# Kernel tuning notes

Measured on AMD Instinct MI355X. Metric: run time of the kernel, lower is better.

The kernel has to match this reference:

```python
import jax, jax.numpy as jnp
import numpy as np

EMB, BS, H = 512, 1024, 8
HD = EMB // H
B, L = 8, 1024
EPS = 1e-5

def setup_inputs() -> dict:
    key = jax.random.key(0)
    ks = jax.random.split(key, 12)
    s = EMB ** -0.5
    return {
        "x": jax.random.normal(ks[0], (B, L, EMB), jnp.float32),
        "ln_g": jnp.ones((EMB,), jnp.float32),
        "ln_b": jnp.zeros((EMB,), jnp.float32),
        "Wq": jax.random.normal(ks[1], (EMB, EMB), jnp.float32) * s,
        "bq": jnp.zeros((EMB,), jnp.float32),
        "Wk": jax.random.normal(ks[2], (EMB, EMB), jnp.float32) * s,
        "bk": jnp.zeros((EMB,), jnp.float32),
        "Wv": jax.random.normal(ks[3], (EMB, EMB), jnp.float32) * s,
        "bv": jnp.zeros((EMB,), jnp.float32),
        "Wo": jax.random.normal(ks[4], (EMB, EMB), jnp.float32) * s,
        "bo": jnp.zeros((EMB,), jnp.float32),
        "Er": jax.random.normal(ks[5], (H, BS, HD), jnp.float32),
    }

def reference(x, ln_g, ln_b, Wq, bq, Wk, bk, Wv, bv, Wo, bo, Er):
    b, l, d = x.shape
    # LayerNorm
    mu = jnp.mean(x, axis=-1, keepdims=True)
    var = jnp.mean((x - mu) ** 2, axis=-1, keepdims=True)
    h = (x - mu) * jax.lax.rsqrt(var + EPS) * ln_g + ln_b
    # projections -> (B, H, L, HD)
    def split_heads(t):
        return t.reshape(b, l, H, HD).transpose(0, 2, 1, 3)
    q = split_heads(h @ Wq + bq)
    k = split_heads(h @ Wk + bk)
    v = split_heads(h @ Wv + bv)
    scores = jnp.einsum('bhld,bhkd->bhlk', q, k) * (HD ** -0.5)
    # relative bias: QEr_all[b,h,l,r] = q . Er[h,r]; then gather r = (k - l) mod BS
    QEr_all = jnp.einsum('bhld,hrd->bhlr', q, Er)  # (B,H,L,BS)
    rel = (jnp.arange(l)[None, :] - jnp.arange(l)[:, None]) % BS  # (L,L), torch negative-index wrap
    QEr = jnp.take_along_axis(QEr_all, rel[None, None], axis=-1)  # (B,H,L,L)
    w = jax.nn.softmax(scores + QEr, axis=-1)
    out = jnp.einsum('bhlk,bhkd->bhld', w, v)
    out = out.transpose(0, 2, 1, 3).reshape(b, l, d)
    return out @ Wo + bo
```

## Files before the change

kernel.cpp:

```cpp
#include <hip/hip_runtime.h>
#include <hip/hip_bf16.h>


typedef __bf16 bf16;
typedef __bf16 bf16x8 __attribute__((ext_vector_type(8)));
typedef float floatx4 __attribute__((ext_vector_type(4)));
typedef float f32x4 __attribute__((ext_vector_type(4)));

#define MFMA16 __builtin_amdgcn_mfma_f32_16x16x32_bf16

#define KS 72
#define PSS 72
#define GS 40
#define TS 72

__global__ __launch_bounds__(256) void prep_ln_kernel(
    const float* __restrict__ Wq, const float* __restrict__ Wk,
    const float* __restrict__ Wv, const float* __restrict__ Wo,
    const float* __restrict__ Er,
    const float* __restrict__ x, const float* __restrict__ g,
    const float* __restrict__ bvec,
    bf16* __restrict__ wt, bf16* __restrict__ er_b, bf16* __restrict__ h) {
  __shared__ __align__(16) bf16 T[64 * TS];
  int blk = blockIdx.x;
  int tid = threadIdx.x;
  if (blk < 256) {
    int w = blk >> 6, rem = blk & 63;
    int r0 = (rem >> 3) << 6, c0 = (rem & 7) << 6;
    const float* W = (w == 0) ? Wq : (w == 1) ? Wk : (w == 2) ? Wv : Wo;
    int row = tid >> 2, cc = (tid & 3) << 4;
    const f32x4* src = (const f32x4*)(W + (r0 + row) * 512 + c0 + cc);
#pragma unroll
    for (int q2 = 0; q2 < 4; q2++) {
      f32x4 v = src[q2];
#pragma unroll
      for (int j = 0; j < 4; j++)
        T[(cc + q2 * 4 + j) * TS + row] = (bf16)v[j];
    }
    __syncthreads();
    int nloc = tid >> 2, kc = (tid & 3) << 4;
    bf16x8 a = *(const bf16x8*)(T + nloc * TS + kc);
    bf16x8 b = *(const bf16x8*)(T + nloc * TS + kc + 8);
    bf16* dst = wt + (w << 18) + (c0 + nloc) * 512 + r0 + kc;
    *(bf16x8*)dst = a;
    *(bf16x8*)(dst + 8) = b;
    return;
  }
  if (blk < 2304) {
    int e = (blk - 256) * 256 + tid;
    er_b[e] = (bf16)Er[e];
    return;
  }
  int row = (blk - 2304) * 4 + (tid >> 6);
  int lane = tid & 63;
  const f32x4* xr = (const f32x4*)(x + row * 512 + lane * 8);
  f32x4 v0 = xr[0], v1 = xr[1];
  float f[8] = {v0[0], v0[1], v0[2], v0[3], v1[0], v1[1], v1[2], v1[3]};
  float s = 0.f, ss = 0.f;
#pragma unroll
  for (int i = 0; i < 8; i++) { s += f[i]; ss += f[i] * f[i]; }
#pragma unroll
  for (int m = 1; m < 64; m <<= 1) { s += __shfl_xor(s, m); ss += __shfl_xor(ss, m); }
  float mean = s * (1.0f / 512.0f);
  float var = ss * (1.0f / 512.0f) - mean * mean;
  float inv = rsqrtf(var + 1e-5f);
  const f32x4* gr = (const f32x4*)(g + lane * 8);
  const f32x4* br = (const f32x4*)(bvec + lane * 8);
  f32x4 g0 = gr[0], g1 = gr[1], b0 = br[0], b1 = br[1];
  float gg[8] = {g0[0], g0[1], g0[2], g0[3], g1[0], g1[1], g1[2], g1[3]};
  float bb[8] = {b0[0], b0[1], b0[2], b0[3], b1[0], b1[1], b1[2], b1[3]};
  bf16x8 o;
#pragma unroll
  for (int i = 0; i < 8; i++)
    o[i] = (bf16)((f[i] - mean) * inv * gg[i] + bb[i]);
  *(bf16x8*)(h + row * 512 + lane * 8) = o;
}


__global__ __launch_bounds__(256) void qkv_gemm(
    const bf16* __restrict__ A,
    const bf16* __restrict__ wt,
    const float* __restrict__ bq, const float* __restrict__ bk,
    const float* __restrict__ bv,
    bf16* __restrict__ q_ws, bf16* __restrict__ k_ws, bf16* __restrict__ vt_ws) {
  __shared__ __align__(16) bf16 smem[64 * 264];
  bf16* As = smem;
  bf16* Bs = smem + 128 * GS;
  int m0 = blockIdx.x * 128;
  int ng0 = blockIdx.y * 128;
  int w = ng0 >> 9;
  int n0 = ng0 & 511;
  const bf16* Bt = wt + (w << 18);
  int tid = threadIdx.x;
  int wave = tid >> 6, lane = tid & 63, quad = lane >> 4, l16 = lane & 15;
  int mq = (wave >> 1) * 64, nq = (wave & 1) * 64;

  floatx4 acc[4][4] = {};
  for (int k0 = 0; k0 < 512; k0 += 32) {
    int r = tid >> 1, c = (tid & 1) * 16;
    *(bf16x8*)(As + r * GS + c)     = *(const bf16x8*)(A + (m0 + r) * 512 + k0 + c);
    *(bf16x8*)(As + r * GS + c + 8) = *(const bf16x8*)(A + (m0 + r) * 512 + k0 + c + 8);
    *(bf16x8*)(Bs + r * GS + c)     = *(const bf16x8*)(Bt + (n0 + r) * 512 + k0 + c);
    *(bf16x8*)(Bs + r * GS + c + 8) = *(const bf16x8*)(Bt + (n0 + r) * 512 + k0 + c + 8);
    __syncthreads();
    bf16x8 a[4], b[4];
#pragma unroll
    for (int mt = 0; mt < 4; mt++)
      a[mt] = *(const bf16x8*)(As + (mq + mt * 16 + l16) * GS + quad * 8);
#pragma unroll
    for (int nt = 0; nt < 4; nt++)
      b[nt] = *(const bf16x8*)(Bs + (nq + nt * 16 + l16) * GS + quad * 8);
#pragma unroll
    for (int mt = 0; mt < 4; mt++)
#pragma unroll
      for (int nt = 0; nt < 4; nt++)
        acc[mt][nt] = MFMA16(a[mt], b[nt], acc[mt][nt], 0, 0, 0);
    __syncthreads();
  }

  if (w == 2) {
#pragma unroll
    for (int nt = 0; nt < 4; nt++) {
      int col = n0 + nq + nt * 16 + l16;
      float bb = bv[col];
      int d = col & 63;
#pragma unroll
      for (int mt = 0; mt < 4; mt++)
#pragma unroll
        for (int r = 0; r < 4; r++) {
          int lloc = mq + mt * 16 + quad * 4 + r;
          smem[d * 264 + (wave & 1) * 128 + lloc] = (bf16)(acc[mt][nt][r] + bb);
        }
    }
    __syncthreads();
    int b_ = m0 >> 10, l0g = m0 & 1023;
    int dloc = tid >> 4, lc = (tid & 15) * 8;
#pragma unroll
    for (int h2 = 0; h2 < 2; h2++) {
      int bh = b_ * 8 + ((n0 + h2 * 64) >> 6);
#pragma unroll
      for (int dd = 0; dd < 4; dd++) {
        int d = dd * 16 + dloc;
        bf16x8 v = *(const bf16x8*)(smem + d * 264 + h2 * 128 + lc);
        *(bf16x8*)(vt_ws + (bh << 16) + (d << 10) + l0g + lc) = v;
      }
    }
    return;
  }

  const float* bias = (w == 0) ? bq : bk;
#pragma unroll
  for (int nt = 0; nt < 4; nt++) {
    int col = n0 + nq + nt * 16 + l16;
    float bb = bias[col];
    int hh = col >> 6, d = col & 63;
#pragma unroll
    for (int mt = 0; mt < 4; mt++) {
#pragma unroll
      for (int r = 0; r < 4; r++) {
        int mrow = m0 + mq + mt * 16 + quad * 4 + r;
        int b_ = mrow >> 10, l = mrow & 1023;
        int bh = b_ * 8 + hh;
        float v = acc[mt][nt][r] + bb;
        if (w == 0) q_ws[(bh << 16) + (l << 6) + d] = (bf16)v;
        else        k_ws[(bh << 16) + (l << 6) + d] = (bf16)(v * 0.125f);
      }
    }
  }
}

__global__ __launch_bounds__(256, 2) void attn_kernel(
    const bf16* __restrict__ q_ws, const bf16* __restrict__ k_ws,
    const bf16* __restrict__ vt_ws, const bf16* __restrict__ Er,
    bf16* __restrict__ o_ws) {
  __shared__ __align__(16) bf16 Ks_s[64 * KS];
  __shared__ __align__(16) bf16 Vs[64 * KS];
  __shared__ __align__(16) bf16 Ers[192 * KS];
  __shared__ __align__(16) bf16 Ps[4][16 * PSS];

  int qt = blockIdx.x;
  int bh = blockIdx.y;
  int hh = bh & 7;
  int l0 = qt << 7;
  int tid = threadIdx.x, wave = tid >> 6, lane = tid & 63;
  int quad = lane >> 4, l16 = lane & 15;

  bf16x8 aq0[2], aq1[2];
#pragma unroll
  for (int strip = 0; strip < 2; strip++) {
    const bf16* qb = q_ws + (bh << 16) + ((l0 + strip * 64 + wave * 16 + l16) << 6);
    aq0[strip] = *(const bf16x8*)(qb + quad * 8);
    aq1[strip] = *(const bf16x8*)(qb + 32 + quad * 8);
  }

  const bf16* kbh = k_ws + (bh << 16);
  const bf16* vbh = vt_ws + (bh << 16);
  const bf16* ebh = Er + (hh << 16);
  bf16* pw = Ps[wave];

  float l_run[2][4] = {};
  floatx4 acc_o[2][4] = {};

  int e0 = -l0 - 127 + 2048;
#pragma unroll
  for (int i = 0; i < 4; i++) {
    int o = tid + i * 256;
    int row = o >> 3, ch = (o & 7) * 8;
    int grow = (e0 + row) & 1023;
    *(bf16x8*)(Ers + row * KS + ch) = *(const bf16x8*)(ebh + (grow << 6) + ch);
  }
  __syncthreads();
  bf16x8 ec0[5], ec1[5];
#pragma unroll
  for (int i = 0; i < 5; i++) {
    int tt = 3 - wave + i;
    const bf16* er = Ers + ((tt << 4) + l16) * KS + quad * 8;
    ec0[i] = *(const bf16x8*)er;
    ec1[i] = *(const bf16x8*)(er + 32);
  }
  int sb = 0;

  for (int kt = 0; kt < 16; kt++) {
    int k0 = kt * 64;
#pragma unroll
    for (int i = 0; i < 2; i++) {
      int o = tid + i * 256;
      int row = o >> 3, ch = (o & 7) * 8;
      *(bf16x8*)(Ks_s + row * KS + ch) =
          *(const bf16x8*)(kbh + ((k0 + row) << 6) + ch);
      *(bf16x8*)(Vs + row * KS + ch) =
          *(const bf16x8*)(vbh + (row << 10) + k0 + ch);
    }
    {
      int s8 = sb + 8; if (s8 >= 12) s8 -= 12;
      int srow0 = s8 << 4;
#pragma unroll
      for (int i = 0; i < 2; i++) {
        int o = tid + i * 256;
        int row = o >> 3, ch = (o & 7) * 8;
        int grow = (e0 + 128 + k0 + row) & 1023;
        *(bf16x8*)(Ers + (srow0 + row) * KS + ch) =
            *(const bf16x8*)(ebh + (grow << 6) + ch);
      }
    }
    __syncthreads();

    bf16x8 kb0[4], kb1[4], vb0[4], vb1[4];
#pragma unroll
    for (int nt = 0; nt < 4; nt++) {
      const bf16* kr = Ks_s + (nt * 16 + l16) * KS + quad * 8;
      kb0[nt] = *(const bf16x8*)kr;
      kb1[nt] = *(const bf16x8*)(kr + 32);
      const bf16* vr = Vs + (nt * 16 + l16) * KS + quad * 8;
      vb0[nt] = *(const bf16x8*)vr;
      vb1[nt] = *(const bf16x8*)(vr + 32);
    }

#pragma unroll
    for (int pass = 0; pass < 2; pass++) {
      int strip = 1 - pass;
      floatx4 acc_s[4] = {};
#pragma unroll
      for (int nt = 0; nt < 4; nt++) {
        acc_s[nt] = MFMA16(aq0[strip], kb0[nt], acc_s[nt], 0, 0, 0);
        acc_s[nt] = MFMA16(aq1[strip], kb1[nt], acc_s[nt], 0, 0, 0);
      }
      floatx4 accb[5];
#pragma unroll
      for (int t = 0; t < 5; t++) {
        floatx4 a = {};
        a = MFMA16(aq0[strip], ec0[t], a, 0, 0, 0);
        a = MFMA16(aq1[strip], ec1[t], a, 0, 0, 0);
        accb[t] = a;
      }
      if (pass == 0) {
#pragma unroll
        for (int i = 0; i < 5; i++) {
          int tt = sb + 7 - wave + i; if (tt >= 12) tt -= 12;
          const bf16* er = Ers + ((tt << 4) + l16) * KS + quad * 8;
          ec0[i] = *(const bf16x8*)er;
          ec1[i] = *(const bf16x8*)(er + 32);
        }
      }
      float pv[4][4];
#pragma unroll
      for (int r = 0; r < 4; r++) {
        int sdl = quad * 4 + r;
        int dd = l16 - sdl;
        int cc = (dd <= 0) ? (15 + dd) : (dd - 1);
        int src = (quad << 4) | cc;
        float rot[5];
#pragma unroll
        for (int t = 0; t < 5; t++) rot[t] = __shfl(accb[t][r], src);
#pragma unroll
        for (int nt = 0; nt < 4; nt++) {
          float b = (dd > 0) ? rot[nt + 1] : rot[nt];
          pv[nt][r] = __expf(acc_s[nt][r] + b);
        }
      }
#pragma unroll
      for (int r = 0; r < 4; r++)
        l_run[strip][r] += pv[0][r] + pv[1][r] + pv[2][r] + pv[3][r];
#pragma unroll
      for (int nt = 0; nt < 4; nt++)
#pragma unroll
        for (int r = 0; r < 4; r++)
          pw[(quad * 4 + r) * PSS + nt * 16 + l16] = (bf16)pv[nt][r];
      bf16x8 ap0 = *(const bf16x8*)(pw + l16 * PSS + quad * 8);
      bf16x8 ap1 = *(const bf16x8*)(pw + l16 * PSS + 32 + quad * 8);
#pragma unroll
      for (int dt = 0; dt < 4; dt++) {
        acc_o[strip][dt] = MFMA16(ap0, vb0[dt], acc_o[strip][dt], 0, 0, 0);
        acc_o[strip][dt] = MFMA16(ap1, vb1[dt], acc_o[strip][dt], 0, 0, 0);
      }
    }
    sb += 4; if (sb >= 12) sb -= 12;
    __syncthreads();
  }

#pragma unroll
  for (int strip = 0; strip < 2; strip++) {
    float invl[4];
#pragma unroll
    for (int r = 0; r < 4; r++) {
      float lr = l_run[strip][r];
#pragma unroll
      for (int m = 1; m < 16; m <<= 1) lr += __shfl_xor(lr, m);
      invl[r] = 1.0f / lr;
    }
#pragma unroll
    for (int dt = 0; dt < 4; dt++) {
      int col = (hh << 6) + dt * 16 + l16;
#pragma unroll
      for (int r = 0; r < 4; r++) {
        int row = ((bh >> 3) << 10) + l0 + strip * 64 + wave * 16 + quad * 4 + r;
        o_ws[row * 512 + col] = (bf16)(acc_o[strip][dt][r] * invl[r]);
      }
    }
  }
}

__global__ __launch_bounds__(256) void out_gemm(
    const bf16* __restrict__ A,
    const bf16* __restrict__ Bt,
    const float* __restrict__ bo, float* __restrict__ out) {
  __shared__ __align__(16) bf16 As[128 * GS];
  __shared__ __align__(16) bf16 Bs[128 * GS];
  int m0 = blockIdx.x * 128;
  int n0 = blockIdx.y * 128;
  int tid = threadIdx.x;
  int wave = tid >> 6, lane = tid & 63, quad = lane >> 4, l16 = lane & 15;
  int mq = (wave >> 1) * 64, nq = (wave & 1) * 64;

  floatx4 acc[4][4] = {};
  for (int k0 = 0; k0 < 512; k0 += 32) {
    int r = tid >> 1, c = (tid & 1) * 16;
    *(bf16x8*)(As + r * GS + c)     = *(const bf16x8*)(A + (m0 + r) * 512 + k0 + c);
    *(bf16x8*)(As + r * GS + c + 8) = *(const bf16x8*)(A + (m0 + r) * 512 + k0 + c + 8);
    *(bf16x8*)(Bs + r * GS + c)     = *(const bf16x8*)(Bt + (n0 + r) * 512 + k0 + c);
    *(bf16x8*)(Bs + r * GS + c + 8) = *(const bf16x8*)(Bt + (n0 + r) * 512 + k0 + c + 8);
    __syncthreads();
    bf16x8 a[4], b[4];
#pragma unroll
    for (int mt = 0; mt < 4; mt++)
      a[mt] = *(const bf16x8*)(As + (mq + mt * 16 + l16) * GS + quad * 8);
#pragma unroll
    for (int nt = 0; nt < 4; nt++)
      b[nt] = *(const bf16x8*)(Bs + (nq + nt * 16 + l16) * GS + quad * 8);
#pragma unroll
    for (int mt = 0; mt < 4; mt++)
#pragma unroll
      for (int nt = 0; nt < 4; nt++)
        acc[mt][nt] = MFMA16(a[mt], b[nt], acc[mt][nt], 0, 0, 0);
    __syncthreads();
  }
#pragma unroll
  for (int nt = 0; nt < 4; nt++) {
    int col = n0 + nq + nt * 16 + l16;
    float bb = bo[col];
#pragma unroll
    for (int mt = 0; mt < 4; mt++) {
#pragma unroll
      for (int r = 0; r < 4; r++) {
        int mrow = m0 + mq + mt * 16 + quad * 4 + r;
        out[mrow * 512 + col] = acc[mt][nt][r] + bb;
      }
    }
  }
}

extern "C" void kernel_launch(void* const* d_in, const int* in_sizes, int n_in,
                              void* d_out, int out_size, void* d_ws, size_t ws_size,
                              hipStream_t stream) {
  const float* x    = (const float*)d_in[0];
  const float* ln_g = (const float*)d_in[1];
  const float* ln_b = (const float*)d_in[2];
  const float* Wq   = (const float*)d_in[3];
  const float* bq   = (const float*)d_in[4];
  const float* Wk   = (const float*)d_in[5];
  const float* bk   = (const float*)d_in[6];
  const float* Wv   = (const float*)d_in[7];
  const float* bv   = (const float*)d_in[8];
  const float* Wo   = (const float*)d_in[9];
  const float* bo   = (const float*)d_in[10];
  const float* Er   = (const float*)d_in[11];
  float* out = (float*)d_out;

  char* ws = (char*)d_ws;
  bf16* wt    = (bf16*)(ws);
  bf16* er_b  = (bf16*)(ws + (2u << 20));
  bf16* h     = (bf16*)(ws + (3u << 20));
  bf16* o_ws  = h;
  bf16* q_ws  = (bf16*)(ws + (11u << 20));
  bf16* k_ws  = (bf16*)(ws + (19u << 20));
  bf16* vt_ws = (bf16*)(ws + (27u << 20));

  prep_ln_kernel<<<4352, 256, 0, stream>>>(Wq, Wk, Wv, Wo, Er, x, ln_g, ln_b,
                                           wt, er_b, h);
  qkv_gemm<<<dim3(64, 12), 256, 0, stream>>>(h, wt, bq, bk, bv, q_ws, k_ws, vt_ws);
  attn_kernel<<<dim3(8, 64), 256, 0, stream>>>(q_ws, k_ws, vt_ws, er_b, o_ws);
  out_gemm<<<dim3(64, 4), 256, 0, stream>>>(o_ws, wt + 3 * 262144, bo, out);
}
```

Measured before the change: 191.6 us.

## Double-buffer K/V tiles and register-prefetch next tile to overlap loads

Loads for the next K, V and Er tiles are now issued into registers while the current tile is being computed. K and V shared-memory tiles are double-buffered so the trailing barrier of each iteration can be removed. This aims to hide global-memory latency behind the MFMA work, at the cost of extra registers (six bf16x8 prefetch values) and more LDS, which may affect occupancy at launch bounds (256,2). Removing the trailing barrier relies on the Er ring-buffer slot being written not overlapping rows still being read by slower waves.

```diff
diff --git a/kernel.cpp b/kernel.cpp
--- a/kernel.cpp
+++ b/kernel.cpp
@@ -173,8 +173,8 @@
     const bf16* __restrict__ q_ws, const bf16* __restrict__ k_ws,
     const bf16* __restrict__ vt_ws, const bf16* __restrict__ Er,
     bf16* __restrict__ o_ws) {
-  __shared__ __align__(16) bf16 Ks_s[64 * KS];
-  __shared__ __align__(16) bf16 Vs[64 * KS];
+  __shared__ __align__(16) bf16 Ks_s[2][64 * KS];
+  __shared__ __align__(16) bf16 Vs[2][64 * KS];
   __shared__ __align__(16) bf16 Ers[192 * KS];
   __shared__ __align__(16) bf16 Ps[4][16 * PSS];
 
@@ -209,6 +209,15 @@
     int grow = (e0 + row) & 1023;
     *(bf16x8*)(Ers + row * KS + ch) = *(const bf16x8*)(ebh + (grow << 6) + ch);
   }
+  int sr0 = tid >> 3, sc0 = (tid & 7) * 8;
+  int sr1 = sr0 + 32;
+  bf16x8 pk[2], pvv[2], pe[2];
+  pk[0]  = *(const bf16x8*)(kbh + (sr0 << 6) + sc0);
+  pk[1]  = *(const bf16x8*)(kbh + (sr1 << 6) + sc0);
+  pvv[0] = *(const bf16x8*)(vbh + (sr0 << 10) + sc0);
+  pvv[1] = *(const bf16x8*)(vbh + (sr1 << 10) + sc0);
+  pe[0]  = *(const bf16x8*)(ebh + (((e0 + 128 + sr0) & 1023) << 6) + sc0);
+  pe[1]  = *(const bf16x8*)(ebh + (((e0 + 128 + sr1) & 1023) << 6) + sc0);
   __syncthreads();
   bf16x8 ec0[5], ec1[5];
 #pragma unroll
@@ -222,38 +231,41 @@
 
   for (int kt = 0; kt < 16; kt++) {
     int k0 = kt * 64;
-#pragma unroll
-    for (int i = 0; i < 2; i++) {
-      int o = tid + i * 256;
-      int row = o >> 3, ch = (o & 7) * 8;
-      *(bf16x8*)(Ks_s + row * KS + ch) =
-          *(const bf16x8*)(kbh + ((k0 + row) << 6) + ch);
-      *(bf16x8*)(Vs + row * KS + ch) =
-          *(const bf16x8*)(vbh + (row << 10) + k0 + ch);
-    }
+    int bsel = kt & 1;
+    bf16* Kb = Ks_s[bsel];
+    bf16* Vb = Vs[bsel];
+    *(bf16x8*)(Kb + sr0 * KS + sc0) = pk[0];
+    *(bf16x8*)(Kb + sr1 * KS + sc0) = pk[1];
+    *(bf16x8*)(Vb + sr0 * KS + sc0) = pvv[0];
+    *(bf16x8*)(Vb + sr1 * KS + sc0) = pvv[1];
     {
       int s8 = sb + 8; if (s8 >= 12) s8 -= 12;
-      int srow0 = s8 << 4;
-#pragma unroll
-      for (int i = 0; i < 2; i++) {
-        int o = tid + i * 256;
-        int row = o >> 3, ch = (o & 7) * 8;
-        int grow = (e0 + 128 + k0 + row) & 1023;
-        *(bf16x8*)(Ers + (srow0 + row) * KS + ch) =
-            *(const bf16x8*)(ebh + (grow << 6) + ch);
-      }
+      bf16* Eb = Ers + (s8 << 4) * KS;
+      *(bf16x8*)(Eb + sr0 * KS + sc0) = pe[0];
+      *(bf16x8*)(Eb + sr1 * KS + sc0) = pe[1];
     }
     __syncthreads();
 
     bf16x8 kb0[4], kb1[4], vb0[4], vb1[4];
 #pragma unroll
     for (int nt = 0; nt < 4; nt++) {
-      const bf16* kr = Ks_s + (nt * 16 + l16) * KS + quad * 8;
+      const bf16* kr = Kb + (nt * 16 + l16) * KS + quad * 8;
       kb0[nt] = *(const bf16x8*)kr;
       kb1[nt] = *(const bf16x8*)(kr + 32);
-      const bf16* vr = Vs + (nt * 16 + l16) * KS + quad * 8;
+      const bf16* vr = Vb + (nt * 16 + l16) * KS + quad * 8;
       vb0[nt] = *(const bf16x8*)vr;
       vb1[nt] = *(const bf16x8*)(vr + 32);
+    }
+
+    {
+      int kn = (kt + 1) & 15;
+      int kn0 = kn * 64;
+      pk[0]  = *(const bf16x8*)(kbh + ((kn0 + sr0) << 6) + sc0);
+      pk[1]  = *(const bf16x8*)(kbh + ((kn0 + sr1) << 6) + sc0);
+      pvv[0] = *(const bf16x8*)(vbh + (sr0 << 10) + kn0 + sc0);
+      pvv[1] = *(const bf16x8*)(vbh + (sr1 << 10) + kn0 + sc0);
+      pe[0]  = *(const bf16x8*)(ebh + (((e0 + 192 + k0 + sr0) & 1023) << 6) + sc0);
+      pe[1]  = *(const bf16x8*)(ebh + (((e0 + 192 + k0 + sr1) & 1023) << 6) + sc0);
     }
 
 #pragma unroll
@@ -315,7 +327,6 @@
       }
     }
     sb += 4; if (sb >= 12) sb -= 12;
-    __syncthreads();
   }
 
 #pragma unroll
```

After: 191.5 us. No clear change (-0.1%).
